# Kernel tuning notes

Measured on AMD Instinct MI355X. Metric: run time of the kernel, lower is better.

The kernel has to match this reference:

```python
import jax, jax.numpy as jnp
import numpy as np

N_NODES = 100000


def sage_conv(x, src, dst, Wl, bl, Wr):
    # PyG SAGEConv (aggr='mean'): out = lin_l(mean_{j in N(i)} x_j) + lin_r(x_i)
    msg = x[src]                                                   # [E, d] gather
    agg = jax.ops.segment_sum(msg, dst, num_segments=N_NODES)      # [N, d]
    cnt = jax.ops.segment_sum(jnp.ones((src.shape[0], 1), x.dtype), dst,
                              num_segments=N_NODES)                # [N, 1]
    mean = agg / jnp.maximum(cnt, 1.0)
    return mean @ Wl + bl + x @ Wr


def setup_inputs() -> dict:
    key = jax.random.key(0)
    ks = jax.random.split(key, 9)
    N, E, D_IN = N_NODES, 3200000, 64
    x = jax.random.normal(ks[0], (N, D_IN), dtype=jnp.float32)
    edge_index = jax.random.randint(ks[1], (2, E), 0, N, dtype=jnp.int64)

    def glorot(k, fan_in, fan_out):
        lim = float(np.sqrt(6.0 / (fan_in + fan_out)))
        return jax.random.uniform(k, (fan_in, fan_out), jnp.float32, -lim, lim)

    return {
        "x": x,
        "edge_index": edge_index,
        "W1l": glorot(ks[2], D_IN, 64), "b1": jnp.zeros((64,), jnp.float32),
        "W1r": glorot(ks[3], D_IN, 64),
        "W2l": glorot(ks[4], 64, 32), "b2": jnp.zeros((32,), jnp.float32),
        "W2r": glorot(ks[5], 64, 32),
        "W3l": glorot(ks[6], 32, 1), "b3": jnp.zeros((1,), jnp.float32),
        "W3r": glorot(ks[7], 32, 1),
    }


def reference(x, edge_index, W1l, b1, W1r, W2l, b2, W2r, W3l, b3, W3r):
    src, dst = edge_index[0], edge_index[1]
    h = jax.nn.relu(sage_conv(x, src, dst, W1l, b1, W1r))   # dropout: eval mode (identity)
    h = jax.nn.relu(sage_conv(h, src, dst, W2l, b2, W2r))
    h = sage_conv(h, src, dst, W3l, b3, W3r)
    return jax.nn.sigmoid(h)                                # [N, 1]
```

## Files before the change

### kernel.cpp

```cpp
#include <hip/hip_runtime.h>
#include <math.h>

#define NN 100000
#define NB 391
#define BT 8192
#define CAP 12288

typedef float vfloat2 __attribute__((ext_vector_type(2)));

__device__ __forceinline__ unsigned short f2bf(float f) {
    unsigned int u = __float_as_uint(f);
    u += 0x7fffu + ((u >> 16) & 1u);
    return (unsigned short)(u >> 16);
}

__device__ __forceinline__ unsigned char f2fp8(float f) {
    const int p = __builtin_amdgcn_cvt_pk_fp8_f32(f, f, 0, false);
    return (unsigned char)(p & 0xFF);
}
template <bool HI>
__device__ __forceinline__ vfloat2 fp8pk2(unsigned int w) {
    return __builtin_amdgcn_cvt_pk_f32_fp8((int)w, HI);
}

template <int D_IN, int D_OUT, int NPB, int FUSE_IN>
__global__ void __launch_bounds__(256)
mlp12_kernel(const float* __restrict__ in0,
             const float* __restrict__ in1,
             const float* __restrict__ Wl,
             const float* __restrict__ Wr,
             const float* __restrict__ bias,
             unsigned char* __restrict__ yout,
             float* __restrict__ zout,
             int n_nodes) {
    constexpr int NG = 256 / D_OUT;
    constexpr int KQ = D_IN / 4;
    __shared__ float sh[NPB * D_IN];
    const int t = threadIdx.x;
    const int node0 = blockIdx.x * NPB;
    for (int i = t; i < NPB * KQ; i += 256) {
        const int ln = i / KQ, kq = i % KQ;
        const int n = node0 + ln;
        float4 v = make_float4(0.f, 0.f, 0.f, 0.f);
        if (n < n_nodes) {
            v = ((const float4*)(in0 + (long long)n * D_IN))[kq];
            if (FUSE_IN) {
                const float4 w = ((const float4*)(in1 + (long long)n * D_IN))[kq];
                v.x = fmaxf(v.x + w.x, 0.f);
                v.y = fmaxf(v.y + w.y, 0.f);
                v.z = fmaxf(v.z + w.z, 0.f);
                v.w = fmaxf(v.w + w.w, 0.f);
            }
        }
        ((float4*)sh)[i] = v;
    }
    const int cc = t % D_OUT;
    const int g = t / D_OUT;
    float wl[D_IN], wr[D_IN];
#pragma unroll
    for (int k = 0; k < D_IN; ++k) {
        wl[k] = Wl[k * D_OUT + cc];
        wr[k] = Wr[k * D_OUT + cc];
    }
    const float badd = bias[cc];
    __syncthreads();
#pragma unroll
    for (int p = 0; p < NPB / NG; ++p) {
        const int ln = g + p * NG;
        const int n = node0 + ln;
        const float4* row = (const float4*)(sh + ln * D_IN);
        float accl = 0.f, accr = 0.f;
#pragma unroll
        for (int kq = 0; kq < KQ; ++kq) {
            const float4 v = row[kq];
            accl += v.x * wl[4 * kq] + v.y * wl[4 * kq + 1] +
                    v.z * wl[4 * kq + 2] + v.w * wl[4 * kq + 3];
            accr += v.x * wr[4 * kq] + v.y * wr[4 * kq + 1] +
                    v.z * wr[4 * kq + 2] + v.w * wr[4 * kq + 3];
        }
        if (n < n_nodes) {
            yout[(long long)n * D_OUT + cc] = f2fp8(accl);
            zout[(long long)n * D_OUT + cc] = accr + badd;
        }
    }
}

template <int D_IN>
__global__ void __launch_bounds__(256)
mlp3_kernel(const float* __restrict__ mean,
            const float* __restrict__ z,
            const float* __restrict__ W3l,
            const float* __restrict__ W3r,
            const float* __restrict__ b3,
            float* __restrict__ y,
            float* __restrict__ z3, int n_nodes) {
    __shared__ float swl[D_IN], swr[D_IN];
    const int t = threadIdx.x;
    if (t < D_IN) { swl[t] = W3l[t]; swr[t] = W3r[t]; }
    __syncthreads();
    const int n = blockIdx.x * 256 + t;
    if (n >= n_nodes) return;
    const float4* pm = (const float4*)(mean + (long long)n * D_IN);
    const float4* pz = (const float4*)(z + (long long)n * D_IN);
    float accl = 0.f, accr = 0.f;
#pragma unroll
    for (int q = 0; q < D_IN / 4; ++q) {
        const float4 m4 = pm[q];
        const float4 z4 = pz[q];
        const float h0 = fmaxf(m4.x + z4.x, 0.f);
        const float h1 = fmaxf(m4.y + z4.y, 0.f);
        const float h2 = fmaxf(m4.z + z4.z, 0.f);
        const float h3 = fmaxf(m4.w + z4.w, 0.f);
        accl += h0 * swl[4 * q] + h1 * swl[4 * q + 1] + h2 * swl[4 * q + 2] + h3 * swl[4 * q + 3];
        accr += h0 * swr[4 * q] + h1 * swr[4 * q + 1] + h2 * swr[4 * q + 2] + h3 * swr[4 * q + 3];
    }
    y[n] = accl;
    z3[n] = accr + b3[0];
}

__global__ void sigmoid_out_kernel(const float* __restrict__ mean,
                                   const float* __restrict__ z,
                                   float* __restrict__ out, int n) {
    const int i = blockIdx.x * 256 + threadIdx.x;
    if (i < n) out[i] = 1.0f / (1.0f + expf(-(mean[i] + z[i])));
}

__global__ void bucket_hist_kernel(const int* __restrict__ dst,
                                   int* __restrict__ bcnt, int n_edges) {
    __shared__ int lh[NB];
    for (int i = threadIdx.x; i < NB; i += 256) lh[i] = 0;
    __syncthreads();
    const int stride = gridDim.x * 256;
    for (int i = blockIdx.x * 256 + threadIdx.x; i < n_edges; i += stride)
        atomicAdd(&lh[dst[i] >> 8], 1);
    __syncthreads();
    for (int i = threadIdx.x; i < NB; i += 256)
        if (lh[i]) atomicAdd(&bcnt[i], lh[i]);
}

__global__ void __launch_bounds__(512)
bucket_scan_kernel(const int* __restrict__ bcnt, int* __restrict__ boffs,
                   int* __restrict__ bcursor) {
    __shared__ int s[512];
    const int t = threadIdx.x;
    const int v = (t < NB) ? bcnt[t] : 0;
    s[t] = v;
    __syncthreads();
    for (int off = 1; off < 512; off <<= 1) {
        const int tmp = (t >= off) ? s[t - off] : 0;
        __syncthreads();
        s[t] += tmp;
        __syncthreads();
    }
    const int excl = s[t] - v;
    if (t <= NB) boffs[t] = excl;
    if (t < NB) bcursor[t] = excl;
}

__global__ void __launch_bounds__(512)
bin_edges_kernel(const int* __restrict__ src, const int* __restrict__ dst,
                 int* __restrict__ bcursor, unsigned int* __restrict__ binned,
                 int n_edges) {
    __shared__ unsigned int stage[BT];
    __shared__ unsigned short sbkt[BT];
    __shared__ int lhist[512], lscan[512], lstart[512], gbase[512], lcur[512];
    const int t = threadIdx.x;
    const int e0 = blockIdx.x * BT;
    const int count = min(BT, n_edges - e0);
    lhist[t] = 0;
    __syncthreads();
    for (int i = t; i < count; i += 512) atomicAdd(&lhist[dst[e0 + i] >> 8], 1);
    __syncthreads();
    const int v = lhist[t];
    lscan[t] = v;
    __syncthreads();
    for (int off = 1; off < 512; off <<= 1) {
        const int tmp = (t >= off) ? lscan[t - off] : 0;
        __syncthreads();
        lscan[t] += tmp;
        __syncthreads();
    }
    const int excl = lscan[t] - v;
    lstart[t] = excl;
    lcur[t] = excl;
    if (t < NB && v > 0) gbase[t] = atomicAdd(&bcursor[t], v);
    __syncthreads();
    for (int i = t; i < count; i += 512) {
        const int d = dst[e0 + i];
        const int b = d >> 8;
        const int p = atomicAdd(&lcur[b], 1);
        stage[p] = (unsigned int)src[e0 + i] | ((unsigned int)(d & 255) << 17);
        sbkt[p] = (unsigned short)b;
    }
    __syncthreads();
    for (int i = t; i < count; i += 512) {
        const int b = sbkt[i];
        binned[gbase[b] + (i - lstart[b])] = stage[i];
    }
}

__global__ void __launch_bounds__(1024)
csr_sort_kernel(const unsigned int* __restrict__ binned,
                const int* __restrict__ boffs,
                int* __restrict__ ssrc, int* __restrict__ row_ptr,
                float* __restrict__ inv_deg, int n_nodes, int n_edges) {
    __shared__ int stage[CAP];
    __shared__ int hist[256];
    __shared__ int lexcl[256];
    __shared__ int lcur[256];
    const int t = threadIdx.x;
    const int b = blockIdx.x;
    const int s0 = boffs[b], s1 = boffs[b + 1];
    const int count = s1 - s0;
    if (t < 256) hist[t] = 0;
    __syncthreads();
    for (int i = t; i < count; i += 1024)
        atomicAdd(&hist[binned[s0 + i] >> 17], 1);
    __syncthreads();
    if (t < 256) lexcl[t] = hist[t];
    __syncthreads();
    for (int off = 1; off < 256; off <<= 1) {
        int tmp = 0;
        if (t < 256 && t >= off) tmp = lexcl[t - off];
        __syncthreads();
        if (t < 256) lexcl[t] += tmp;
        __syncthreads();
    }
    if (t < 256) {
        const int excl = lexcl[t] - hist[t];
        lcur[t] = excl;
        const int n = (b << 8) + t;
        if (n < n_nodes) {
            row_ptr[n] = s0 + excl;
            inv_deg[n] = 1.0f / (float)max(hist[t], 1);
        }
    }
    if (b == NB - 1 && t == 0) row_ptr[n_nodes] = n_edges;
    __syncthreads();
    for (int i = t; i < count; i += 1024) {
        const unsigned int v = binned[s0 + i];
        const int p = atomicAdd(&lcur[v >> 17], 1);
        if (p < CAP) stage[p] = (int)(v & 0x1FFFFu);
    }
    __syncthreads();
    for (int i = t; i < count; i += 1024) ssrc[s0 + i] = stage[i];
}

template <int D>
__global__ void agg_mean_fp8_kernel(const unsigned int* __restrict__ yb,
                                    const int* __restrict__ row_ptr,
                                    const int* __restrict__ ssrc,
                                    const float* __restrict__ inv_deg,
                                    float* __restrict__ mean, int n_nodes) {
    constexpr int G = D / 16;
    constexpr int NPB = 256 / G;
    const int g = threadIdx.x / G;
    const int lane = threadIdx.x % G;
    const int n = blockIdx.x * NPB + g;
    if (n >= n_nodes) return;
    const int s0 = row_ptr[n], s1 = row_ptr[n + 1];
    const uint4* yv = (const uint4*)yb;
    float acc[16];
#pragma unroll
    for (int i = 0; i < 16; ++i) acc[i] = 0.f;
    int e = s0;
    for (; e + 4 <= s1; e += 4) {
        uint4 v[4];
        v[0] = yv[(long long)ssrc[e] * G + lane];
        v[1] = yv[(long long)ssrc[e + 1] * G + lane];
        v[2] = yv[(long long)ssrc[e + 2] * G + lane];
        v[3] = yv[(long long)ssrc[e + 3] * G + lane];
#pragma unroll
        for (int q = 0; q < 4; ++q) {
            const unsigned int wx = v[q].x, wy = v[q].y, wz = v[q].z, ww = v[q].w;
            vfloat2 p;
            p = fp8pk2<false>(wx); acc[0]  += p.x; acc[1]  += p.y;
            p = fp8pk2<true>(wx);  acc[2]  += p.x; acc[3]  += p.y;
            p = fp8pk2<false>(wy); acc[4]  += p.x; acc[5]  += p.y;
            p = fp8pk2<true>(wy);  acc[6]  += p.x; acc[7]  += p.y;
            p = fp8pk2<false>(wz); acc[8]  += p.x; acc[9]  += p.y;
            p = fp8pk2<true>(wz);  acc[10] += p.x; acc[11] += p.y;
            p = fp8pk2<false>(ww); acc[12] += p.x; acc[13] += p.y;
            p = fp8pk2<true>(ww);  acc[14] += p.x; acc[15] += p.y;
        }
    }
    for (; e < s1; ++e) {
        const uint4 v = yv[(long long)ssrc[e] * G + lane];
        vfloat2 p;
        p = fp8pk2<false>(v.x); acc[0]  += p.x; acc[1]  += p.y;
        p = fp8pk2<true>(v.x);  acc[2]  += p.x; acc[3]  += p.y;
        p = fp8pk2<false>(v.y); acc[4]  += p.x; acc[5]  += p.y;
        p = fp8pk2<true>(v.y);  acc[6]  += p.x; acc[7]  += p.y;
        p = fp8pk2<false>(v.z); acc[8]  += p.x; acc[9]  += p.y;
        p = fp8pk2<true>(v.z);  acc[10] += p.x; acc[11] += p.y;
        p = fp8pk2<false>(v.w); acc[12] += p.x; acc[13] += p.y;
        p = fp8pk2<true>(v.w);  acc[14] += p.x; acc[15] += p.y;
    }
    const float inv = inv_deg[n];
    float4* mv = (float4*)mean;
    const long long base = (long long)n * (D / 4) + lane * 4;
#pragma unroll
    for (int q = 0; q < 4; ++q)
        mv[base + q] = make_float4(acc[4 * q] * inv, acc[4 * q + 1] * inv,
                                   acc[4 * q + 2] * inv, acc[4 * q + 3] * inv);
}

__global__ void agg_mean_d1_kernel(const float* __restrict__ y,
                                   const int* __restrict__ row_ptr,
                                   const int* __restrict__ ssrc,
                                   const float* __restrict__ inv_deg,
                                   float* __restrict__ mean, int n_nodes) {
    const int wave = threadIdx.x >> 6;
    const int lane = threadIdx.x & 63;
    const int n = blockIdx.x * 4 + wave;
    if (n >= n_nodes) return;
    const int s0 = row_ptr[n], s1 = row_ptr[n + 1];
    float acc = 0.f;
    for (int e = s0 + lane; e < s1; e += 64) acc += y[ssrc[e]];
    for (int off = 32; off > 0; off >>= 1) acc += __shfl_down(acc, off, 64);
    if (lane == 0) mean[n] = acc * inv_deg[n];
}

extern "C" void kernel_launch(void* const* d_in, const int* in_sizes, int n_in,
                              void* d_out, int out_size, void* d_ws, size_t ws_size,
                              hipStream_t stream) {
    const float* x = (const float*)d_in[0];
    const int* edge_index = (const int*)d_in[1];
    const float* W1l = (const float*)d_in[2];
    const float* b1  = (const float*)d_in[3];
    const float* W1r = (const float*)d_in[4];
    const float* W2l = (const float*)d_in[5];
    const float* b2  = (const float*)d_in[6];
    const float* W2r = (const float*)d_in[7];
    const float* W3l = (const float*)d_in[8];
    const float* b3  = (const float*)d_in[9];
    const float* W3r = (const float*)d_in[10];
    float* out = (float*)d_out;

    const int E = in_sizes[1] / 2;
    const int* src = edge_index;
    const int* dst = edge_index + E;

    float* bufY    = (float*)d_ws;
    float* meanB   = bufY + 32LL * NN;
    float* z1      = meanB + 64LL * NN;
    float* z2      = z1 + 64LL * NN;
    float* z3      = z2 + 32LL * NN;
    float* inv_deg = z3 + NN;
    int* bcnt      = (int*)(inv_deg + NN);
    int* boffs     = bcnt + NB;
    int* bcursor   = boffs + NB + 1;
    int* row_ptr   = bcursor + NB;
    int* ssrc      = row_ptr + NN + 1;
    unsigned int* binned = (unsigned int*)z1;

    const int ntiles = (E + BT - 1) / BT;

    (void)hipMemsetAsync(bcnt, 0, NB * sizeof(int), stream);
    bucket_hist_kernel<<<512, 256, 0, stream>>>(dst, bcnt, E);
    bucket_scan_kernel<<<1, 512, 0, stream>>>(bcnt, boffs, bcursor);
    bin_edges_kernel<<<ntiles, 512, 0, stream>>>(src, dst, bcursor, binned, E);
    csr_sort_kernel<<<NB, 1024, 0, stream>>>(binned, boffs, ssrc, row_ptr, inv_deg, NN, E);

    mlp12_kernel<64, 64, 16, 0><<<(NN + 15) / 16, 256, 0, stream>>>(
        x, nullptr, W1l, W1r, b1, (unsigned char*)bufY, z1, NN);
    agg_mean_fp8_kernel<64><<<(NN + 63) / 64, 256, 0, stream>>>(
        (const unsigned int*)bufY, row_ptr, ssrc, inv_deg, meanB, NN);

    mlp12_kernel<64, 32, 16, 1><<<(NN + 15) / 16, 256, 0, stream>>>(
        meanB, z1, W2l, W2r, b2, (unsigned char*)bufY, z2, NN);
    agg_mean_fp8_kernel<32><<<(NN + 127) / 128, 256, 0, stream>>>(
        (const unsigned int*)bufY, row_ptr, ssrc, inv_deg, meanB, NN);

    mlp3_kernel<32><<<(NN + 255) / 256, 256, 0, stream>>>(
        meanB, z2, W3l, W3r, b3, bufY, z3, NN);
    agg_mean_d1_kernel<<<(NN + 3) / 4, 256, 0, stream>>>(
        bufY, row_ptr, ssrc, inv_deg, meanB, NN);
    sigmoid_out_kernel<<<(NN + 255) / 256, 256, 0, stream>>>(meanB, z3, out, NN);
}
```

Measured before the change: 349.1 us.

## Use bf16 MFMA for fused dense layers with larger node tiles

Replaces the scalar-FMA per-node dense transform for layers 1 and 2 with a kernel that converts inputs and concatenated Wl/Wr weights to bf16 in shared memory in MFMA fragment layout and uses 16x16x32 bf16 matrix instructions. Each block now handles 128 nodes instead of 16, so the weight staging cost is amortised over more nodes. This lowers precision of the linear layers to bf16 inputs, and the output stores are scattered byte/float writes per accumulator row.

```diff
diff --git a/kernel.cpp b/kernel.cpp
--- a/kernel.cpp
+++ b/kernel.cpp
@@ -7,6 +7,8 @@
 #define CAP 12288
 
 typedef float vfloat2 __attribute__((ext_vector_type(2)));
+typedef short short8 __attribute__((ext_vector_type(8)));
+typedef float floatx4 __attribute__((ext_vector_type(4)));
 
 __device__ __forceinline__ unsigned short f2bf(float f) {
     unsigned int u = __float_as_uint(f);
@@ -23,64 +25,103 @@
     return __builtin_amdgcn_cvt_pk_f32_fp8((int)w, HI);
 }
 
-template <int D_IN, int D_OUT, int NPB, int FUSE_IN>
+template <int D_IN, int CL, int CR, int NPB, int FUSE_IN>
 __global__ void __launch_bounds__(256)
-mlp12_kernel(const float* __restrict__ in0,
-             const float* __restrict__ in1,
-             const float* __restrict__ Wl,
-             const float* __restrict__ Wr,
-             const float* __restrict__ bias,
-             unsigned char* __restrict__ yout,
-             float* __restrict__ zout,
-             int n_nodes) {
-    constexpr int NG = 256 / D_OUT;
-    constexpr int KQ = D_IN / 4;
-    __shared__ float sh[NPB * D_IN];
+mlp_mfma_kernel(const float* __restrict__ in0,
+                const float* __restrict__ in1,
+                const float* __restrict__ Wl,
+                const float* __restrict__ Wr,
+                const float* __restrict__ bias,
+                unsigned char* __restrict__ yout,
+                float* __restrict__ zout,
+                int n_nodes) {
+    constexpr int COLS = CL + CR;
+    constexpr int CT = COLS / 16;
+    constexpr int KT = D_IN / 32;
+    constexpr int NT = NPB / 16;
+    constexpr int KG = D_IN / 8;
+    __shared__ short sA[NT * KT * 64 * 8];
+    __shared__ short sB[CT * KT * 64 * 8];
+    __shared__ float sBias[CR];
     const int t = threadIdx.x;
     const int node0 = blockIdx.x * NPB;
-    for (int i = t; i < NPB * KQ; i += 256) {
-        const int ln = i / KQ, kq = i % KQ;
-        const int n = node0 + ln;
-        float4 v = make_float4(0.f, 0.f, 0.f, 0.f);
+
+    for (int i = t; i < NPB * KG; i += 256) {
+        const int nl = i / KG, kg = i % KG;
+        const int n = node0 + nl;
+        float v[8];
         if (n < n_nodes) {
-            v = ((const float4*)(in0 + (long long)n * D_IN))[kq];
+            const float4* p = (const float4*)(in0 + (long long)n * D_IN + kg * 8);
+            float4 a0 = p[0], a1 = p[1];
             if (FUSE_IN) {
-                const float4 w = ((const float4*)(in1 + (long long)n * D_IN))[kq];
-                v.x = fmaxf(v.x + w.x, 0.f);
-                v.y = fmaxf(v.y + w.y, 0.f);
-                v.z = fmaxf(v.z + w.z, 0.f);
-                v.w = fmaxf(v.w + w.w, 0.f);
+                const float4* q = (const float4*)(in1 + (long long)n * D_IN + kg * 8);
+                const float4 b0 = q[0], b1 = q[1];
+                a0.x = fmaxf(a0.x + b0.x, 0.f); a0.y = fmaxf(a0.y + b0.y, 0.f);
+                a0.z = fmaxf(a0.z + b0.z, 0.f); a0.w = fmaxf(a0.w + b0.w, 0.f);
+                a1.x = fmaxf(a1.x + b1.x, 0.f); a1.y = fmaxf(a1.y + b1.y, 0.f);
+                a1.z = fmaxf(a1.z + b1.z, 0.f); a1.w = fmaxf(a1.w + b1.w, 0.f);
             }
+            v[0] = a0.x; v[1] = a0.y; v[2] = a0.z; v[3] = a0.w;
+            v[4] = a1.x; v[5] = a1.y; v[6] = a1.z; v[7] = a1.w;
+        } else {
+#pragma unroll
+            for (int j = 0; j < 8; ++j) v[j] = 0.f;
         }
-        ((float4*)sh)[i] = v;
-    }
-    const int cc = t % D_OUT;
-    const int g = t / D_OUT;
-    float wl[D_IN], wr[D_IN];
-#pragma unroll
-    for (int k = 0; k < D_IN; ++k) {
-        wl[k] = Wl[k * D_OUT + cc];
-        wr[k] = Wr[k * D_OUT + cc];
-    }
-    const float badd = bias[cc];
-    __syncthreads();
-#pragma unroll
-    for (int p = 0; p < NPB / NG; ++p) {
-        const int ln = g + p * NG;
-        const int n = node0 + ln;
-        const float4* row = (const float4*)(sh + ln * D_IN);
-        float accl = 0.f, accr = 0.f;
-#pragma unroll
-        for (int kq = 0; kq < KQ; ++kq) {
-            const float4 v = row[kq];
-            accl += v.x * wl[4 * kq] + v.y * wl[4 * kq + 1] +
-                    v.z * wl[4 * kq + 2] + v.w * wl[4 * kq + 3];
-            accr += v.x * wr[4 * kq] + v.y * wr[4 * kq + 1] +
-                    v.z * wr[4 * kq + 2] + v.w * wr[4 * kq + 3];
+        short8 s;
+#pragma unroll
+        for (int j = 0; j < 8; ++j) s[j] = (short)f2bf(v[j]);
+        const int nt = nl >> 4, m = nl & 15, kt = kg >> 2, quad = kg & 3;
+        ((short8*)sA)[(nt * KT + kt) * 64 + quad * 16 + m] = s;
+    }
+    for (int i = t; i < CT * KT * 64; i += 256) {
+        const int ct = i / (KT * 64);
+        const int rem = i % (KT * 64);
+        const int kt = rem / 64, L = rem % 64;
+        const int c = ct * 16 + (L & 15);
+        const int k0 = kt * 32 + (L >> 4) * 8;
+        short8 s;
+#pragma unroll
+        for (int j = 0; j < 8; ++j) {
+            const int k = k0 + j;
+            const float w = (c < CL) ? Wl[k * CL + c] : Wr[k * CR + (c - CL)];
+            s[j] = (short)f2bf(w);
         }
-        if (n < n_nodes) {
-            yout[(long long)n * D_OUT + cc] = f2fp8(accl);
-            zout[(long long)n * D_OUT + cc] = accr + badd;
+        ((short8*)sB)[i] = s;
+    }
+    for (int i = t; i < CR; i += 256) sBias[i] = bias[i];
+    __syncthreads();
+
+    const int w = t >> 6, lane = t & 63;
+    short8 Bf[CT][KT];
+#pragma unroll
+    for (int ct = 0; ct < CT; ++ct)
+#pragma unroll
+        for (int kt = 0; kt < KT; ++kt)
+            Bf[ct][kt] = ((short8*)sB)[(ct * KT + kt) * 64 + lane];
+    const int col = lane & 15, quad = lane >> 4;
+#pragma unroll
+    for (int nti = 0; nti < NT / 4; ++nti) {
+        const int nt = w * (NT / 4) + nti;
+        short8 A[KT];
+#pragma unroll
+        for (int kt = 0; kt < KT; ++kt)
+            A[kt] = ((short8*)sA)[(nt * KT + kt) * 64 + lane];
+        const int nodeb = node0 + nt * 16 + quad * 4;
+#pragma unroll
+        for (int ct = 0; ct < CT; ++ct) {
+            floatx4 acc = {0.f, 0.f, 0.f, 0.f};
+#pragma unroll
+            for (int kt = 0; kt < KT; ++kt)
+                acc = __builtin_amdgcn_mfma_f32_16x16x32_bf16(A[kt], Bf[ct][kt], acc, 0, 0, 0);
+            const int gc = ct * 16 + col;
+#pragma unroll
+            for (int r = 0; r < 4; ++r) {
+                const int node = nodeb + r;
+                if (node < n_nodes) {
+                    if (gc < CL) yout[(long long)node * CL + gc] = f2fp8(acc[r]);
+                    else zout[(long long)node * CR + (gc - CL)] = acc[r] + sBias[gc - CL];
+                }
+            }
         }
     }
 }
@@ -362,12 +403,12 @@
     bin_edges_kernel<<<ntiles, 512, 0, stream>>>(src, dst, bcursor, binned, E);
     csr_sort_kernel<<<NB, 1024, 0, stream>>>(binned, boffs, ssrc, row_ptr, inv_deg, NN, E);
 
-    mlp12_kernel<64, 64, 16, 0><<<(NN + 15) / 16, 256, 0, stream>>>(
+    mlp_mfma_kernel<64, 64, 64, 128, 0><<<(NN + 127) / 128, 256, 0, stream>>>(
         x, nullptr, W1l, W1r, b1, (unsigned char*)bufY, z1, NN);
     agg_mean_fp8_kernel<64><<<(NN + 63) / 64, 256, 0, stream>>>(
         (const unsigned int*)bufY, row_ptr, ssrc, inv_deg, meanB, NN);
 
-    mlp12_kernel<64, 32, 16, 1><<<(NN + 15) / 16, 256, 0, stream>>>(
+    mlp_mfma_kernel<64, 32, 32, 128, 1><<<(NN + 127) / 128, 256, 0, stream>>>(
         meanB, z1, W2l, W2r, b2, (unsigned char*)bufY, z2, NN);
     agg_mean_fp8_kernel<32><<<(NN + 127) / 128, 256, 0, stream>>>(
         (const unsigned int*)bufY, row_ptr, ssrc, inv_deg, meanB, NN);
```

After: 301.8 us. -13.5%, faster.
